# Kernel tuning notes

Measured on AMD Instinct MI355X. Metric: run time of the kernel, lower is better.

## Reference

```python
import jax, jax.numpy as jnp
import numpy as np

NUM_HEAD = 16
MASKED_BIAS = -10000.0


def setup_inputs() -> dict:
    key = jax.random.key(0)
    k1, k2, k3 = jax.random.split(key, 3)
    B, M, N = 2, 2048, 1024
    x = jax.random.normal(k1, (B, M, N), dtype=jnp.float32)
    w_attn = jax.random.normal(k2, (N, 3 * N), dtype=jnp.float32) * 0.02
    w_proj = jax.random.normal(k3, (N, N), dtype=jnp.float32) * 0.02
    b_attn = jnp.zeros((3 * N,), dtype=jnp.float32)
    b_proj = jnp.zeros((N,), dtype=jnp.float32)
    return {"x": x, "w_attn": w_attn, "w_proj": w_proj,
            "b_attn": b_attn, "b_proj": b_proj}


def reference(x, w_attn, w_proj, b_attn, b_proj):
    B, M, N = x.shape
    H = NUM_HEAD
    d = N // H  # head dim
    # fused QKV projection: [B,M,3N]
    qkv = jnp.einsum('bmn,nd->bmd', x, w_attn) + b_attn
    q, k, v = jnp.split(qkv, 3, axis=-1)
    # split heads -> [B,H,M,d]
    q = q.reshape(B, M, H, d).transpose(0, 2, 1, 3)
    k = k.reshape(B, M, H, d).transpose(0, 2, 1, 3)
    v = v.reshape(B, M, H, d).transpose(0, 2, 1, 3)
    # scaled dot-product scores [B,H,M,M]
    scores = jnp.einsum('bhqd,bhkd->bhqk', q, k) / jnp.sqrt(jnp.float32(d))
    causal = jnp.tril(jnp.ones((M, M), dtype=bool))  # GPT-2 bias buffer
    scores = jnp.where(causal, scores, jnp.float32(MASKED_BIAS))
    attn = jax.nn.softmax(scores, axis=-1)
    # context [B,H,M,d] -> [B,M,N]
    ctx = jnp.einsum('bhqk,bhkd->bhqd', attn, v)
    ctx = ctx.transpose(0, 2, 1, 3).reshape(B, M, N)
    # output projection
    out = jnp.einsum('bmn,no->bmo', ctx, w_proj) + b_proj
    return out
```

## Files before the change

### kernel.cpp

```cpp
#include <hip/hip_runtime.h>

typedef __attribute__((ext_vector_type(8))) __bf16 bf16x8;
typedef __attribute__((ext_vector_type(4))) __bf16 bf16x4;
typedef __attribute__((ext_vector_type(4))) float f32x4;

__device__ __forceinline__ void async_copy16(const void* g, void* l) {
    __builtin_amdgcn_global_load_lds(
        (const __attribute__((address_space(1))) void*)g,
        (__attribute__((address_space(3))) void*)l, 16, 0, 0);
}

__global__ __launch_bounds__(256) void cast_bf16_k(
    const float* __restrict__ src, __bf16* __restrict__ dst)
{
    size_t i = ((size_t)blockIdx.x * 256 + threadIdx.x) * 8;
    float4 a = *(const float4*)&src[i];
    float4 b = *(const float4*)&src[i + 4];
    bf16x8 o;
    o[0] = (__bf16)a.x; o[1] = (__bf16)a.y; o[2] = (__bf16)a.z; o[3] = (__bf16)a.w;
    o[4] = (__bf16)b.x; o[5] = (__bf16)b.y; o[6] = (__bf16)b.z; o[7] = (__bf16)b.w;
    *(bf16x8*)&dst[i] = o;
}

__global__ __launch_bounds__(256) void transpose_cast_k(
    const float* __restrict__ src, __bf16* __restrict__ dst, int R, int C)
{
    __shared__ float tile[32][33];
    int c0 = blockIdx.x * 32, r0 = blockIdx.y * 32;
    int tx = threadIdx.x & 31, ty = threadIdx.x >> 5;
    for (int i = ty; i < 32; i += 8)
        tile[i][tx] = src[(size_t)(r0 + i) * C + (c0 + tx)];
    __syncthreads();
    for (int i = ty; i < 32; i += 8)
        dst[(size_t)(c0 + i) * R + (r0 + tx)] = (__bf16)tile[tx][i];
}

template <int MODE, int TN>
__global__ __launch_bounds__(256) void gemm_bt(
    const __bf16* __restrict__ A, const __bf16* __restrict__ Bt,
    const float* __restrict__ bias, int K,
    __bf16* __restrict__ O0, __bf16* __restrict__ O1, __bf16* __restrict__ O2,
    float* __restrict__ Of)
{
    constexpr int NJ = TN / 32;
    __shared__ __align__(16) __bf16 lds_a[128 * 32];
    __shared__ __align__(16) __bf16 lds_b[TN * 32];
    const int row0 = blockIdx.x * 128;
    const int col0 = blockIdx.y * TN;
    const int tid  = threadIdx.x;
    const int lane = tid & 63;
    const int w    = tid >> 6;
    const int wm   = (w >> 1) * 64, wn = (w & 1) * (TN / 2);
    const int quad = lane >> 4, l16 = lane & 15;

    f32x4 acc[4][NJ] = {};
    for (int kb = 0; kb < K; kb += 32) {
#pragma unroll
        for (int t = 0; t < 2; ++t) {
            int s = t * 256 + tid;
            int L = s >> 3, c = (s & 7) ^ (L & 7);
            int row = 2 * L + (c >> 2), ch = c & 3;
            async_copy16(&A[(size_t)(row0 + row) * K + kb + ch * 8],
                         (char*)lds_a + (t * 256 + w * 64) * 16);
        }
#pragma unroll
        for (int t = 0; t < TN / 64; ++t) {
            int s = t * 256 + tid;
            int L = s >> 3, c = (s & 7) ^ (L & 7);
            int row = 2 * L + (c >> 2), ch = c & 3;
            async_copy16(&Bt[(size_t)(col0 + row) * K + kb + ch * 8],
                         (char*)lds_b + (t * 256 + w * 64) * 16);
        }
        __syncthreads();
        bf16x8 af[4], bfr[NJ];
#pragma unroll
        for (int i = 0; i < 4; ++i) {
            int r = wm + i * 16 + l16;
            int L = r >> 1, g = ((r & 1) * 4 + quad) ^ (L & 7);
            af[i] = *(const bf16x8*)&lds_a[L * 64 + g * 8];
        }
#pragma unroll
        for (int j = 0; j < NJ; ++j) {
            int r = wn + j * 16 + l16;
            int L = r >> 1, g = ((r & 1) * 4 + quad) ^ (L & 7);
            bfr[j] = *(const bf16x8*)&lds_b[L * 64 + g * 8];
        }
#pragma unroll
        for (int i = 0; i < 4; ++i)
#pragma unroll
            for (int j = 0; j < NJ; ++j)
                acc[i][j] = __builtin_amdgcn_mfma_f32_16x16x32_bf16(
                    af[i], bfr[j], acc[i][j], 0, 0, 0);
        __syncthreads();
    }

#pragma unroll
    for (int i = 0; i < 4; ++i) {
        int grow = row0 + wm + i * 16 + quad * 4;
#pragma unroll
        for (int j = 0; j < NJ; ++j) {
            int gcol = col0 + wn + j * 16 + l16;
            float bv = bias[gcol];
            if constexpr (MODE == 0) {
                int which = gcol >> 10;
                int n  = gcol & 1023;
                int hh = n >> 6, dd = n & 63;
                int bb = grow >> 11, mm0 = grow & 2047;
                int bhh = bb * 16 + hh;
                if (which == 2) {
                    bf16x4 pk;
#pragma unroll
                    for (int r = 0; r < 4; ++r)
                        pk[r] = (__bf16)(acc[i][j][r] + bv);
                    *(bf16x4*)&O2[((size_t)bhh * 64 + dd) * 2048 + mm0] = pk;
                } else {
#pragma unroll
                    for (int r = 0; r < 4; ++r) {
                        float v = acc[i][j][r] + bv;
                        if (which == 0)
                            O0[((size_t)bhh * 2048 + mm0 + r) * 64 + dd] =
                                (__bf16)(v * 0.18033688011112042f);
                        else
                            O1[((size_t)bhh * 2048 + mm0 + r) * 64 + dd] =
                                (__bf16)v;
                    }
                }
            } else {
#pragma unroll
                for (int r = 0; r < 4; ++r) {
                    int gr = grow + r;
                    Of[(size_t)gr * 1024 + gcol] = acc[i][j][r] + bv;
                }
            }
        }
    }
}

__global__ __launch_bounds__(256) void attn_kernel(
    const __bf16* __restrict__ Qh, const __bf16* __restrict__ Kh,
    const __bf16* __restrict__ Vt, __bf16* __restrict__ ctx)
{
    const int M = 2048, D = 64;
    const int bh = blockIdx.x;
    const int qt = 31 - blockIdx.y;
    const int b = bh >> 4, h = bh & 15;
    const int tid = threadIdx.x, lane = tid & 63, w = tid >> 6;
    const int quad = lane >> 4, l16 = lane & 15;

    const int q0 = qt * 64;
    const int nIter = qt + 1;

    __shared__ __align__(16) __bf16 lds_k[2][64 * 64];
    __shared__ __align__(16) __bf16 lds_v[2][64 * 64];
    __shared__ __align__(16) __bf16 lds_p[4][16 * 72];

    const __bf16* Qp = Qh + (size_t)bh * M * D;
    const __bf16* Kp = Kh + (size_t)bh * M * D;
    const __bf16* Vp = Vt + (size_t)bh * D * M;

    const int qbase = q0 + w * 16;

    bf16x8 qf[2];
#pragma unroll
    for (int c = 0; c < 2; ++c)
        qf[c] = *(const bf16x8*)
            &Qp[(size_t)(qbase + l16) * D + c * 32 + quad * 8];

    f32x4 acc[4] = {};
    f32x4 acc_s = {};
    const __bf16 onev = (__bf16)1.0f;
    const bf16x8 ones = {onev, onev, onev, onev, onev, onev, onev, onev};

    auto stage = [&](int pb, int kb) {
#pragma unroll
        for (int t = 0; t < 2; ++t) {
            int c = w * 128 + t * 64 + lane;
            int row = c >> 3, ch = c & 7;
            int gch = ch ^ (row & 7);
            async_copy16(&Kp[(size_t)(kb + row) * 64 + gch * 8],
                         (char*)&lds_k[pb][0] + (w * 128 + t * 64) * 16);
            async_copy16(&Vp[(size_t)row * M + kb + gch * 8],
                         (char*)&lds_v[pb][0] + (w * 128 + t * 64) * 16);
        }
    };

    stage(0, 0);
    __bf16* pl = &lds_p[w][0];

    for (int it = 0; it < nIter; ++it) {
        const int kb = it << 6;
        __syncthreads();
        if (it + 1 < nIter) stage((it + 1) & 1, kb + 64);
        const __bf16* kt = &lds_k[it & 1][0];
        const __bf16* vt = &lds_v[it & 1][0];

        f32x4 s[4];
#pragma unroll
        for (int j = 0; j < 4; ++j) {
            f32x4 t = {};
#pragma unroll
            for (int c = 0; c < 2; ++c) {
                int ch = ((c << 2) + quad) ^ (l16 & 7);
                bf16x8 kf = *(const bf16x8*)
                    &kt[(((j << 4) + l16) << 6) + (ch << 3)];
                t = __builtin_amdgcn_mfma_f32_16x16x32_bf16(
                    qf[c], kf, t, 0, 0, 0);
            }
            s[j] = t;
        }
        if (kb + 63 > qbase) {
#pragma unroll
            for (int j = 0; j < 4; ++j)
#pragma unroll
                for (int r = 0; r < 4; ++r)
                    if (kb + j * 16 + l16 > qbase + quad * 4 + r)
                        s[j][r] = -1e30f;
        }
#pragma unroll
        for (int j = 0; j < 4; ++j)
#pragma unroll
            for (int r = 0; r < 4; ++r)
                s[j][r] = exp2f(s[j][r]);
#pragma unroll
        for (int j = 0; j < 4; ++j)
#pragma unroll
            for (int r = 0; r < 4; ++r)
                pl[(quad * 4 + r) * 72 + j * 16 + l16] = (__bf16)s[j][r];
        bf16x8 pf[2];
#pragma unroll
        for (int c = 0; c < 2; ++c)
            pf[c] = *(const bf16x8*)&pl[l16 * 72 + c * 32 + quad * 8];
#pragma unroll
        for (int f = 0; f < 4; ++f)
#pragma unroll
            for (int c = 0; c < 2; ++c) {
                int ch = ((c << 2) + quad) ^ (l16 & 7);
                bf16x8 vf = *(const bf16x8*)
                    &vt[(((f << 4) + l16) << 6) + (ch << 3)];
                acc[f] = __builtin_amdgcn_mfma_f32_16x16x32_bf16(
                    pf[c], vf, acc[f], 0, 0, 0);
            }
#pragma unroll
        for (int c = 0; c < 2; ++c)
            acc_s = __builtin_amdgcn_mfma_f32_16x16x32_bf16(
                pf[c], ones, acc_s, 0, 0, 0);
    }

#pragma unroll
    for (int f = 0; f < 4; ++f)
#pragma unroll
        for (int r = 0; r < 4; ++r) {
            int q = qbase + quad * 4 + r;
            int col = h * 64 + f * 16 + l16;
            ctx[((size_t)(b * 2048 + q)) * 1024 + col] =
                (__bf16)(acc[f][r] / acc_s[r]);
        }
}

extern "C" void kernel_launch(void* const* d_in, const int* in_sizes, int n_in,
                              void* d_out, int out_size, void* d_ws, size_t ws_size,
                              hipStream_t stream) {
    const float* x      = (const float*)d_in[0];
    const float* w_attn = (const float*)d_in[1];
    const float* w_proj = (const float*)d_in[2];
    const float* b_attn = (const float*)d_in[3];
    const float* b_proj = (const float*)d_in[4];
    float* out = (float*)d_out;

    char* ws = (char*)d_ws;
    __bf16* xb  = (__bf16*)(ws);
    __bf16* ctx = (__bf16*)(ws);
    __bf16* wAt = (__bf16*)(ws + 8388608);
    __bf16* wPt = (__bf16*)(ws + 14680064);
    __bf16* Vt  = (__bf16*)(ws + 16777216);
    __bf16* Qh  = (__bf16*)d_out;
    __bf16* Kh  = (__bf16*)d_out + 4194304;

    cast_bf16_k<<<2048, 256, 0, stream>>>(x, xb);
    transpose_cast_k<<<dim3(96, 32), 256, 0, stream>>>(w_attn, wAt, 1024, 3072);
    transpose_cast_k<<<dim3(32, 32), 256, 0, stream>>>(w_proj, wPt, 1024, 1024);
    gemm_bt<0, 128><<<dim3(32, 24), 256, 0, stream>>>(xb, wAt, b_attn, 1024,
                                                      Qh, Kh, Vt, nullptr);
    attn_kernel<<<dim3(32, 32), 256, 0, stream>>>(Qh, Kh, Vt, ctx);
    gemm_bt<1, 64><<<dim3(32, 16), 256, 0, stream>>>(ctx, wPt, b_proj, 1024,
                                                     nullptr, nullptr, nullptr, out);
}
```

Baseline: 188.1 us.

## Keep attention probabilities in registers via transposed MFMA, fuse prep kernels

The attention kernel now computes S^T (K as the A operand) so each lane's exp'd scores directly form the B operand of a 16x16x16 MFMA for P·V. This removes the per-iteration LDS round trip for P, along with its shared buffer. The output is staged through LDS for coalesced 16-byte ctx stores. The three cast/transpose prep kernels are merged into one launch to cut launch overhead. The trade-off is that PV now uses twice as many smaller MFMAs with 8-byte V reads, and the row sum is taken from acc_s[0], which relies on the transposed layout.

```diff
diff --git a/kernel.cpp b/kernel.cpp
--- a/kernel.cpp
+++ b/kernel.cpp
@@ -3,6 +3,7 @@
 typedef __attribute__((ext_vector_type(8))) __bf16 bf16x8;
 typedef __attribute__((ext_vector_type(4))) __bf16 bf16x4;
 typedef __attribute__((ext_vector_type(4))) float f32x4;
+typedef __attribute__((ext_vector_type(4))) short short4v;
 
 __device__ __forceinline__ void async_copy16(const void* g, void* l) {
     __builtin_amdgcn_global_load_lds(
@@ -10,23 +11,33 @@
         (__attribute__((address_space(3))) void*)l, 16, 0, 0);
 }
 
-__global__ __launch_bounds__(256) void cast_bf16_k(
-    const float* __restrict__ src, __bf16* __restrict__ dst)
-{
-    size_t i = ((size_t)blockIdx.x * 256 + threadIdx.x) * 8;
-    float4 a = *(const float4*)&src[i];
-    float4 b = *(const float4*)&src[i + 4];
-    bf16x8 o;
-    o[0] = (__bf16)a.x; o[1] = (__bf16)a.y; o[2] = (__bf16)a.z; o[3] = (__bf16)a.w;
-    o[4] = (__bf16)b.x; o[5] = (__bf16)b.y; o[6] = (__bf16)b.z; o[7] = (__bf16)b.w;
-    *(bf16x8*)&dst[i] = o;
-}
-
-__global__ __launch_bounds__(256) void transpose_cast_k(
-    const float* __restrict__ src, __bf16* __restrict__ dst, int R, int C)
+__global__ __launch_bounds__(256) void prep_k(
+    const float* __restrict__ x, __bf16* __restrict__ xb,
+    const float* __restrict__ wa, __bf16* __restrict__ wAt,
+    const float* __restrict__ wp, __bf16* __restrict__ wPt)
 {
     __shared__ float tile[32][33];
-    int c0 = blockIdx.x * 32, r0 = blockIdx.y * 32;
+    const int bx = blockIdx.x;
+    if (bx < 2048) {
+        size_t i = ((size_t)bx * 256 + threadIdx.x) * 8;
+        float4 a = *(const float4*)&x[i];
+        float4 b = *(const float4*)&x[i + 4];
+        bf16x8 o;
+        o[0] = (__bf16)a.x; o[1] = (__bf16)a.y; o[2] = (__bf16)a.z; o[3] = (__bf16)a.w;
+        o[4] = (__bf16)b.x; o[5] = (__bf16)b.y; o[6] = (__bf16)b.z; o[7] = (__bf16)b.w;
+        *(bf16x8*)&xb[i] = o;
+        return;
+    }
+    const float* src; __bf16* dst; int R, C, c0, r0;
+    if (bx < 5120) {
+        int id = bx - 2048;
+        src = wa; dst = wAt; R = 1024; C = 3072;
+        c0 = (id % 96) * 32; r0 = (id / 96) * 32;
+    } else {
+        int id = bx - 5120;
+        src = wp; dst = wPt; R = 1024; C = 1024;
+        c0 = (id & 31) * 32; r0 = (id >> 5) * 32;
+    }
     int tx = threadIdx.x & 31, ty = threadIdx.x >> 5;
     for (int i = ty; i < 32; i += 8)
         tile[i][tx] = src[(size_t)(r0 + i) * C + (c0 + tx)];
@@ -152,24 +163,22 @@
 
     __shared__ __align__(16) __bf16 lds_k[2][64 * 64];
     __shared__ __align__(16) __bf16 lds_v[2][64 * 64];
-    __shared__ __align__(16) __bf16 lds_p[4][16 * 72];
 
     const __bf16* Qp = Qh + (size_t)bh * M * D;
     const __bf16* Kp = Kh + (size_t)bh * M * D;
     const __bf16* Vp = Vt + (size_t)bh * D * M;
 
-    const int qbase = q0 + w * 16;
+    const int qw = q0 + w * 16;
 
     bf16x8 qf[2];
 #pragma unroll
     for (int c = 0; c < 2; ++c)
         qf[c] = *(const bf16x8*)
-            &Qp[(size_t)(qbase + l16) * D + c * 32 + quad * 8];
-
-    f32x4 acc[4] = {};
+            &Qp[(size_t)(qw + l16) * D + c * 32 + quad * 8];
+
+    f32x4 acc2[4] = {};
     f32x4 acc_s = {};
-    const __bf16 onev = (__bf16)1.0f;
-    const bf16x8 ones = {onev, onev, onev, onev, onev, onev, onev, onev};
+    const short4v ones2 = {0x3F80, 0x3F80, 0x3F80, 0x3F80};
 
     auto stage = [&](int pb, int kb) {
 #pragma unroll
@@ -185,7 +194,6 @@
     };
 
     stage(0, 0);
-    __bf16* pl = &lds_p[w][0];
 
     for (int it = 0; it < nIter; ++it) {
         const int kb = it << 6;
@@ -196,65 +204,72 @@
 
         f32x4 s[4];
 #pragma unroll
-        for (int j = 0; j < 4; ++j) {
-            f32x4 t = {};
+        for (int t = 0; t < 4; ++t) {
+            f32x4 tt = {};
 #pragma unroll
             for (int c = 0; c < 2; ++c) {
                 int ch = ((c << 2) + quad) ^ (l16 & 7);
                 bf16x8 kf = *(const bf16x8*)
-                    &kt[(((j << 4) + l16) << 6) + (ch << 3)];
-                t = __builtin_amdgcn_mfma_f32_16x16x32_bf16(
-                    qf[c], kf, t, 0, 0, 0);
+                    &kt[(((t << 4) + l16) << 6) + (ch << 3)];
+                tt = __builtin_amdgcn_mfma_f32_16x16x32_bf16(
+                    kf, qf[c], tt, 0, 0, 0);
             }
-            s[j] = t;
-        }
-        if (kb + 63 > qbase) {
-#pragma unroll
-            for (int j = 0; j < 4; ++j)
+            s[t] = tt;
+        }
+        if (kb + 63 > qw) {
+#pragma unroll
+            for (int t = 0; t < 4; ++t)
 #pragma unroll
                 for (int r = 0; r < 4; ++r)
-                    if (kb + j * 16 + l16 > qbase + quad * 4 + r)
-                        s[j][r] = -1e30f;
-        }
-#pragma unroll
-        for (int j = 0; j < 4; ++j)
+                    if (kb + t * 16 + quad * 4 + r > qw + l16)
+                        s[t][r] = -1e30f;
+        }
+        short4v pf[4];
+#pragma unroll
+        for (int t = 0; t < 4; ++t) {
+            bf16x4 pk;
 #pragma unroll
             for (int r = 0; r < 4; ++r)
-                s[j][r] = exp2f(s[j][r]);
-#pragma unroll
-        for (int j = 0; j < 4; ++j)
-#pragma unroll
-            for (int r = 0; r < 4; ++r)
-                pl[(quad * 4 + r) * 72 + j * 16 + l16] = (__bf16)s[j][r];
-        bf16x8 pf[2];
-#pragma unroll
-        for (int c = 0; c < 2; ++c)
-            pf[c] = *(const bf16x8*)&pl[l16 * 72 + c * 32 + quad * 8];
+                pk[r] = (__bf16)exp2f(s[t][r]);
+            pf[t] = *(short4v*)&pk;
+        }
 #pragma unroll
         for (int f = 0; f < 4; ++f)
 #pragma unroll
-            for (int c = 0; c < 2; ++c) {
-                int ch = ((c << 2) + quad) ^ (l16 & 7);
-                bf16x8 vf = *(const bf16x8*)
-                    &vt[(((f << 4) + l16) << 6) + (ch << 3)];
-                acc[f] = __builtin_amdgcn_mfma_f32_16x16x32_bf16(
-                    pf[c], vf, acc[f], 0, 0, 0);
+            for (int t = 0; t < 4; ++t) {
+                int row = (f << 4) + l16;
+                int g = ((t << 1) + (quad >> 1)) ^ (row & 7);
+                bf16x4 vv = *(const bf16x4*)
+                    &vt[(row << 6) + (g << 3) + ((quad & 1) << 2)];
+                acc2[f] = __builtin_amdgcn_mfma_f32_16x16x16bf16_1k(
+                    *(short4v*)&vv, pf[t], acc2[f], 0, 0, 0);
             }
 #pragma unroll
-        for (int c = 0; c < 2; ++c)
-            acc_s = __builtin_amdgcn_mfma_f32_16x16x32_bf16(
-                pf[c], ones, acc_s, 0, 0, 0);
-    }
-
-#pragma unroll
-    for (int f = 0; f < 4; ++f)
-#pragma unroll
-        for (int r = 0; r < 4; ++r) {
-            int q = qbase + quad * 4 + r;
-            int col = h * 64 + f * 16 + l16;
-            ctx[((size_t)(b * 2048 + q)) * 1024 + col] =
-                (__bf16)(acc[f][r] / acc_s[r]);
-        }
+        for (int t = 0; t < 4; ++t)
+            acc_s = __builtin_amdgcn_mfma_f32_16x16x16bf16_1k(
+                ones2, pf[t], acc_s, 0, 0, 0);
+    }
+
+    __syncthreads();
+    __bf16* ldsT = &lds_k[0][0];
+    const float l = acc_s[0];
+#pragma unroll
+    for (int f = 0; f < 4; ++f) {
+        bf16x4 ov;
+#pragma unroll
+        for (int r = 0; r < 4; ++r)
+            ov[r] = (__bf16)(acc2[f][r] / l);
+        *(bf16x4*)&ldsT[(w * 16 + l16) * 72 + f * 16 + quad * 4] = ov;
+    }
+    __syncthreads();
+    {
+        int qq = tid >> 2;
+        int dp = (tid & 3) * 16;
+        const __bf16* src = &ldsT[qq * 72 + dp];
+        __bf16* dst = &ctx[((size_t)(b * 2048 + q0 + qq)) * 1024 + h * 64 + dp];
+        *(bf16x8*)&dst[0] = *(const bf16x8*)&src[0];
+        *(bf16x8*)&dst[8] = *(const bf16x8*)&src[8];
+    }
 }
 
 extern "C" void kernel_launch(void* const* d_in, const int* in_sizes, int n_in,
@@ -276,9 +291,7 @@
     __bf16* Qh  = (__bf16*)d_out;
     __bf16* Kh  = (__bf16*)d_out + 4194304;
 
-    cast_bf16_k<<<2048, 256, 0, stream>>>(x, xb);
-    transpose_cast_k<<<dim3(96, 32), 256, 0, stream>>>(w_attn, wAt, 1024, 3072);
-    transpose_cast_k<<<dim3(32, 32), 256, 0, stream>>>(w_proj, wPt, 1024, 1024);
+    prep_k<<<6144, 256, 0, stream>>>(x, xb, w_attn, wAt, w_proj, wPt);
     gemm_bt<0, 128><<<dim3(32, 24), 256, 0, stream>>>(xb, wAt, b_attn, 1024,
                                                       Qh, Kh, Vt, nullptr);
     attn_kernel<<<dim3(32, 32), 256, 0, stream>>>(Qh, Kh, Vt, ctx);
```

Result: faster. 183.8 us (-2.3%).
